# Kernel optimization log

Hardware: AMD Instinct MI355X
Metric: run time of the kernel (lower is better)

## Reference

```python
import jax, jax.numpy as jnp
import numpy as np

V, E, H, B, S = 32000, 128, 256, 8, 512


def setup_inputs() -> dict:
    key = jax.random.key(0)
    ks = jax.random.split(key, 8)
    s_cell = 1.0 / np.sqrt(H)
    return {
        "t": jax.random.randint(ks[0], (B, S), 0, V),
        "emb": jax.random.normal(ks[1], (V, E), dtype=jnp.float32) * 0.02,
        "h0": jnp.zeros((1, H), dtype=jnp.float32),
        "w_ih": jax.random.uniform(ks[2], (3 * H, E), jnp.float32, -s_cell, s_cell),
        "w_hh": jax.random.uniform(ks[3], (3 * H, H), jnp.float32, -s_cell, s_cell),
        "b_ih": jax.random.uniform(ks[4], (3 * H,), jnp.float32, -s_cell, s_cell),
        "b_hh": jax.random.uniform(ks[5], (3 * H,), jnp.float32, -s_cell, s_cell),
        "w_out": jax.random.normal(ks[6], (V, H), dtype=jnp.float32) * 0.02,
        "b_out": jnp.zeros((V,), dtype=jnp.float32),
    }


def reference(t, emb, h0, w_ih, w_hh, b_ih, b_hh, w_out, b_out):
    x = emb[t]  # [B, S, E]
    # Input-side gate pre-activations can be batched over time (same math as per-step GRUCell)
    gi = jnp.einsum("bse,ge->bsg", x, w_ih) + b_ih  # [B, S, 3H]
    h_init = jnp.broadcast_to(h0, (t.shape[0], h0.shape[1]))  # [B, H]

    def step(h, gi_t):  # gi_t: [B, 3H]
        gh = h @ w_hh.T + b_hh  # [B, 3H]
        i_r, i_z, i_n = jnp.split(gi_t, 3, axis=-1)
        h_r, h_z, h_n = jnp.split(gh, 3, axis=-1)
        r = jax.nn.sigmoid(i_r + h_r)
        z = jax.nn.sigmoid(i_z + h_z)
        n = jnp.tanh(i_n + r * h_n)
        h_new = (1.0 - z) * n + z * h
        return h_new, h_new

    _, hs = jax.lax.scan(step, h_init, jnp.swapaxes(gi, 0, 1))  # hs: [S, B, H]
    hidden = jnp.swapaxes(hs, 0, 1)  # [B, S, H]
    return jnp.einsum("bsh,vh->bsv", hidden, w_out) + b_out  # [B, S, V]
```

## Files before the change

### kernel.cpp

```cpp
#include <hip/hip_runtime.h>
#include <stdint.h>


typedef __attribute__((ext_vector_type(8))) _Float16 half8;
typedef __attribute__((ext_vector_type(4))) _Float16 half4;
typedef __attribute__((ext_vector_type(4))) float float4v;
typedef __attribute__((ext_vector_type(4))) float facc4;
typedef __attribute__((ext_vector_type(4))) unsigned short ushort4v;

#define GI_BYTES   (512 * 8 * 768 * 4)
#define HID_BYTES  (4096 * 256 * 2)
#define FLAG_OFF   (GI_BYTES + HID_BYTES)

__device__ __forceinline__ float b2f(unsigned short u) {
  union { unsigned int i; float f; } v; v.i = ((unsigned int)u) << 16; return v.f;
}
__device__ __forceinline__ unsigned short f2b(float f) {
  union { float f; unsigned int i; } v; v.f = f;
  unsigned int r = v.i + 0x7FFFu + ((v.i >> 16) & 1u);
  return (unsigned short)(r >> 16);
}
template<bool BF> __device__ __forceinline__ float ldf(const void* p, int i) {
  if constexpr (BF) return b2f(((const unsigned short*)p)[i]);
  else              return ((const float*)p)[i];
}
template<bool BF> __device__ __forceinline__ float4v ld4(const void* p, int i) {
  float4v r;
  if constexpr (BF) {
    ushort4v u = *reinterpret_cast<const ushort4v*>((const unsigned short*)p + i);
#pragma unroll
    for (int j = 0; j < 4; ++j) r[j] = b2f(u[j]);
  } else {
    r = *reinterpret_cast<const float4v*>((const float*)p + i);
  }
  return r;
}

__global__ void k_detect(const unsigned int* __restrict__ emb_raw,
                         int* __restrict__ flag) {
  int tid = threadIdx.x;
  unsigned int u = emb_raw[tid];
  unsigned int lo = u & 0xFFFFu;
  unsigned int ex = (lo >> 7) & 0xFFu;
  int hit = ((ex >= 96u && ex <= 127u) || lo == 0u) ? 1 : 0;
  unsigned long long m = __ballot(hit);
  if (tid == 0) flag[0] = (__popcll(m) >= 40) ? 1 : 0;
}

template<bool BF>
__global__ __launch_bounds__(256, 4) void k_gi(
    const int* __restrict__ flag, const int* __restrict__ t,
    const void* __restrict__ emb, const void* __restrict__ w_ih,
    const void* __restrict__ b_ih, float* __restrict__ gi)
{
  if (*flag != (BF ? 1 : 0)) return;
  alignas(16) __shared__ float x_lds[4][128];
  const int n0 = blockIdx.x * 4;
  const int tid = threadIdx.x;
  for (int i = tid; i < 512; i += 256) {
    int tk = i >> 7, e = i & 127;
    int n = n0 + tk, s = n >> 3, b = n & 7;
    int tok = t[b * 512 + s];
    x_lds[tk][e] = ldf<BF>(emb, tok * 128 + e);
  }
  __syncthreads();
#pragma unroll
  for (int gg = 0; gg < 3; ++gg) {
    int g = gg * 256 + tid;
    float bias = ldf<BF>(b_ih, g);
    float a0 = bias, a1 = bias, a2 = bias, a3 = bias;
    for (int kb = 0; kb < 32; ++kb) {
      float4v w4 = ld4<BF>(w_ih, g * 128 + kb * 4);
#pragma unroll
      for (int j = 0; j < 4; ++j) {
        float w = w4[j]; int k = kb * 4 + j;
        a0 = fmaf(w, x_lds[0][k], a0);
        a1 = fmaf(w, x_lds[1][k], a1);
        a2 = fmaf(w, x_lds[2][k], a2);
        a3 = fmaf(w, x_lds[3][k], a3);
      }
    }
    gi[(n0 + 0) * 768 + g] = a0;
    gi[(n0 + 1) * 768 + g] = a1;
    gi[(n0 + 2) * 768 + g] = a2;
    gi[(n0 + 3) * 768 + g] = a3;
  }
}

template<bool BF>
__global__ __launch_bounds__(1024, 4) void k_scan(
    const int* __restrict__ flag, const void* __restrict__ w_hh,
    const void* __restrict__ b_hh, const void* __restrict__ h0,
    const float* __restrict__ gi, _Float16* __restrict__ hidden)
{
  if (*flag != (BF ? 1 : 0)) return;
  alignas(16) __shared__ _Float16 a_sh[2][256];
  alignas(16) __shared__ float gi_sh[2][768];
  alignas(16) __shared__ float bhh_sh[768];

  const int tid = threadIdx.x;
  const int b = blockIdx.x;
  const int wave = tid >> 6, lane = tid & 63;
  const int l15 = lane & 15, q = lane >> 4;
  const bool ard = (l15 == 0);
  const int qo = q * 8;

  half8 bfr[3][8];
#pragma unroll
  for (int tt = 0; tt < 3; ++tt) {
    int nrow = tt * 256 + (wave << 4) + l15;
#pragma unroll
    for (int kt = 0; kt < 8; ++kt) {
      int base = nrow * 256 + kt * 32 + qo;
      float4v x0 = ld4<BF>(w_hh, base), x1 = ld4<BF>(w_hh, base + 4);
      half8 h;
#pragma unroll
      for (int jj = 0; jj < 4; ++jj) { h[jj] = (_Float16)x0[jj]; h[4 + jj] = (_Float16)x1[jj]; }
      bfr[tt][kt] = h;
    }
  }

  if (tid < 768) bhh_sh[tid] = ldf<BF>(b_hh, tid);
  if (tid < 256) a_sh[0][tid] = (_Float16)ldf<BF>(h0, tid);
  if (tid < 768) gi_sh[0][tid] = gi[b * 768 + tid];
  float hreg = 0.f;
  if (lane < 16) hreg = ldf<BF>(h0, (wave << 4) + lane);

  half8 a0 = {}, a1 = {};
  _Float16* hid = hidden + b * 512 * 256;
  __syncthreads();

  int p = 0;
  for (int s = 0; s < 512; ++s) {
    float gnext = 0.f;
    if (tid < 768 && s < 511) gnext = gi[(s + 1) * 6144 + b * 768 + tid];

    const _Float16* ap = &a_sh[p][0];
    facc4 acc0 = {}, acc1 = {}, acc2 = {};
    if (ard) a0 = *reinterpret_cast<const half8*>(ap + qo);
#pragma unroll
    for (int kt = 0; kt < 8; kt += 2) {
      if (ard) a1 = *reinterpret_cast<const half8*>(ap + (kt + 1) * 32 + qo);
      acc0 = __builtin_amdgcn_mfma_f32_16x16x32_f16(a0, bfr[0][kt], acc0, 0, 0, 0);
      acc1 = __builtin_amdgcn_mfma_f32_16x16x32_f16(a0, bfr[1][kt], acc1, 0, 0, 0);
      acc2 = __builtin_amdgcn_mfma_f32_16x16x32_f16(a0, bfr[2][kt], acc2, 0, 0, 0);
      if (ard && kt + 2 < 8) a0 = *reinterpret_cast<const half8*>(ap + (kt + 2) * 32 + qo);
      acc0 = __builtin_amdgcn_mfma_f32_16x16x32_f16(a1, bfr[0][kt + 1], acc0, 0, 0, 0);
      acc1 = __builtin_amdgcn_mfma_f32_16x16x32_f16(a1, bfr[1][kt + 1], acc1, 0, 0, 0);
      acc2 = __builtin_amdgcn_mfma_f32_16x16x32_f16(a1, bfr[2][kt + 1], acc2, 0, 0, 0);
    }

    if (tid < 768 && s < 511) gi_sh[p ^ 1][tid] = gnext;

    if (lane < 16) {
      int j = (wave << 4) + lane;
      float ghr = acc0[0] + bhh_sh[j];
      float ghz = acc1[0] + bhh_sh[256 + j];
      float ghn = acc2[0] + bhh_sh[512 + j];
      float gir = gi_sh[p][j], giz = gi_sh[p][256 + j], gin = gi_sh[p][512 + j];
      float r = 1.f / (1.f + __expf(-(gir + ghr)));
      float z = 1.f / (1.f + __expf(-(giz + ghz)));
      float xn = gin + r * ghn;
      float e2 = __expf(2.f * xn);
      float nn = 1.f - 2.f / (e2 + 1.f);
      float hnew = (1.f - z) * nn + z * hreg;
      hreg = hnew;
      _Float16 hf = (_Float16)hnew;
      a_sh[p ^ 1][j] = hf;
      hid[s * 256 + j] = hf;
    }
    __syncthreads();
    p ^= 1;
  }
}

template<bool BF>
__global__ __launch_bounds__(256, 2) void k_out(
    const int* __restrict__ flag, const _Float16* __restrict__ hidden,
    const void* __restrict__ w_out, const void* __restrict__ b_out,
    void* __restrict__ out)
{
  if (*flag != (BF ? 1 : 0)) return;
  alignas(16) __shared__ _Float16 Asm[128 * 72];
  alignas(16) __shared__ _Float16 Bsm[128 * 72];
  const int bid = blockIdx.x;
  const int m0 = (bid & 31) * 128;
  const int n0 = (bid >> 5) * 128;
  const int tid = threadIdx.x;
  const int wave = tid >> 6, lane = tid & 63;
  const int l15 = lane & 15, q = lane >> 4;
  const int wm = (wave >> 1) * 64, wn = (wave & 1) * 64;

  facc4 acc[4][4] = {};
  float bo[4];
#pragma unroll
  for (int nt = 0; nt < 4; ++nt)
    bo[nt] = ldf<BF>(b_out, n0 + wn + nt * 16 + l15);

  for (int kk = 0; kk < 4; ++kk) {
    int k0 = kk * 64;
#pragma unroll
    for (int r = 0; r < 4; ++r) {
      int row = r * 32 + (tid >> 3);
      int ch = tid & 7;
      *reinterpret_cast<half8*>(&Asm[row * 72 + ch * 8]) =
          *reinterpret_cast<const half8*>(hidden + (m0 + row) * 256 + k0 + ch * 8);
      int wbase = (n0 + row) * 256 + k0 + ch * 8;
      float4v w0 = ld4<BF>(w_out, wbase), w1 = ld4<BF>(w_out, wbase + 4);
      half8 hB;
#pragma unroll
      for (int j = 0; j < 4; ++j) { hB[j] = (_Float16)w0[j]; hB[4 + j] = (_Float16)w1[j]; }
      *reinterpret_cast<half8*>(&Bsm[row * 72 + ch * 8]) = hB;
    }
    __syncthreads();
#pragma unroll
    for (int kt = 0; kt < 2; ++kt) {
      int koff = kt * 32 + q * 8;
      half8 af[4], bf[4];
#pragma unroll
      for (int mt = 0; mt < 4; ++mt)
        af[mt] = *reinterpret_cast<const half8*>(&Asm[(wm + mt * 16 + l15) * 72 + koff]);
#pragma unroll
      for (int nt = 0; nt < 4; ++nt)
        bf[nt] = *reinterpret_cast<const half8*>(&Bsm[(wn + nt * 16 + l15) * 72 + koff]);
#pragma unroll
      for (int mt = 0; mt < 4; ++mt)
#pragma unroll
        for (int nt = 0; nt < 4; ++nt)
          acc[mt][nt] = __builtin_amdgcn_mfma_f32_16x16x32_f16(
              af[mt], bf[nt], acc[mt][nt], 0, 0, 0);
    }
    __syncthreads();
  }
#pragma unroll
  for (int mt = 0; mt < 4; ++mt) {
#pragma unroll
    for (int i = 0; i < 4; ++i) {
      int row = m0 + wm + mt * 16 + q * 4 + i;
#pragma unroll
      for (int nt = 0; nt < 4; ++nt) {
        int col = n0 + wn + nt * 16 + l15;
        float val = acc[mt][nt][i] + bo[nt];
        if constexpr (BF) ((unsigned short*)out)[row * 32000 + col] = f2b(val);
        else              ((float*)out)[row * 32000 + col] = val;
      }
    }
  }
}

extern "C" void kernel_launch(void* const* d_in, const int* in_sizes, int n_in,
                              void* d_out, int out_size, void* d_ws, size_t ws_size,
                              hipStream_t stream) {
  const int* t     = (const int*)d_in[0];
  const void* emb  = d_in[1];
  const void* h0   = d_in[2];
  const void* w_ih = d_in[3];
  const void* w_hh = d_in[4];
  const void* b_ih = d_in[5];
  const void* b_hh = d_in[6];
  const void* w_out = d_in[7];
  const void* b_out = d_in[8];

  float*     gi     = (float*)d_ws;
  _Float16*  hidden = (_Float16*)((char*)d_ws + GI_BYTES);
  int*       flag   = (int*)((char*)d_ws + FLAG_OFF);

  k_detect<<<1, 64, 0, stream>>>((const unsigned int*)emb, flag);

  k_gi<false><<<1024, 256, 0, stream>>>(flag, t, emb, w_ih, b_ih, gi);
  k_gi<true> <<<1024, 256, 0, stream>>>(flag, t, emb, w_ih, b_ih, gi);

  k_scan<false><<<8, 1024, 0, stream>>>(flag, w_hh, b_hh, h0, gi, hidden);
  k_scan<true> <<<8, 1024, 0, stream>>>(flag, w_hh, b_hh, h0, gi, hidden);

  k_out<false><<<8000, 256, 0, stream>>>(flag, hidden, w_out, b_out, d_out);
  k_out<true> <<<8000, 256, 0, stream>>>(flag, hidden, w_out, b_out, d_out);
}
```

Baseline: 1.533 ms.

## Restructure GRU scan step: register gi/bias, LDS ring for hidden, lighter barrier

The scan kernel now keeps gate inputs and recurrent biases in registers instead of staging them through shared memory. It seeds the MFMA accumulators with the bias and writes hidden states into a 32-deep LDS ring. Hidden-state global stores are batched as coalesced half4 writes every 16 steps, and the per-step __syncthreads is replaced by an explicit lgkmcnt wait plus s_barrier. The aim is a shorter serial critical path per timestep. The output GEMM also remaps block indices for XCD locality, and removing the occupancy hint on the scan kernel may change register allocation.

New measurement: 2.109 ms. 37.6% more time.

```diff
diff --git a/kernel.cpp b/kernel.cpp
--- a/kernel.cpp
+++ b/kernel.cpp
@@ -34,6 +34,14 @@
     r = *reinterpret_cast<const float4v*>((const float*)p + i);
   }
   return r;
+}
+
+__device__ __forceinline__ void bar_lgkm() {
+  __builtin_amdgcn_sched_barrier(0);
+  asm volatile("s_waitcnt lgkmcnt(0)" ::: "memory");
+  __builtin_amdgcn_sched_barrier(0);
+  __builtin_amdgcn_s_barrier();
+  __builtin_amdgcn_sched_barrier(0);
 }
 
 __global__ void k_detect(const unsigned int* __restrict__ emb_raw,
@@ -88,27 +96,25 @@
 }
 
 template<bool BF>
-__global__ __launch_bounds__(1024, 4) void k_scan(
+__global__ __launch_bounds__(1024) void k_scan(
     const int* __restrict__ flag, const void* __restrict__ w_hh,
     const void* __restrict__ b_hh, const void* __restrict__ h0,
     const float* __restrict__ gi, _Float16* __restrict__ hidden)
 {
   if (*flag != (BF ? 1 : 0)) return;
-  alignas(16) __shared__ _Float16 a_sh[2][256];
-  alignas(16) __shared__ float gi_sh[2][768];
-  alignas(16) __shared__ float bhh_sh[768];
+  alignas(16) __shared__ _Float16 hs[32][256];
 
   const int tid = threadIdx.x;
   const int b = blockIdx.x;
   const int wave = tid >> 6, lane = tid & 63;
   const int l15 = lane & 15, q = lane >> 4;
-  const bool ard = (l15 == 0);
   const int qo = q * 8;
+  const int j = (wave << 4) + l15;
 
   half8 bfr[3][8];
 #pragma unroll
   for (int tt = 0; tt < 3; ++tt) {
-    int nrow = tt * 256 + (wave << 4) + l15;
+    int nrow = tt * 256 + j;
 #pragma unroll
     for (int kt = 0; kt < 8; ++kt) {
       int base = nrow * 256 + kt * 32 + qo;
@@ -120,57 +126,68 @@
     }
   }
 
-  if (tid < 768) bhh_sh[tid] = ldf<BF>(b_hh, tid);
-  if (tid < 256) a_sh[0][tid] = (_Float16)ldf<BF>(h0, tid);
-  if (tid < 768) gi_sh[0][tid] = gi[b * 768 + tid];
-  float hreg = 0.f;
-  if (lane < 16) hreg = ldf<BF>(h0, (wave << 4) + lane);
-
-  half8 a0 = {}, a1 = {};
+  const float bh_r = ldf<BF>(b_hh, j);
+  const float bh_z = ldf<BF>(b_hh, 256 + j);
+  const float bh_n = ldf<BF>(b_hh, 512 + j);
+
+  if (tid < 256) hs[31][tid] = (_Float16)ldf<BF>(h0, tid);
+  float hreg = (lane < 16) ? ldf<BF>(h0, j) : 0.f;
+
+  float gr_c = 0.f, gz_c = 0.f, gn_c = 0.f;
+  if (lane < 16) {
+    const float* g0 = gi + b * 768 + j;
+    gr_c = g0[0]; gz_c = g0[256]; gn_c = g0[512];
+  }
+  __syncthreads();
+
   _Float16* hid = hidden + b * 512 * 256;
-  __syncthreads();
-
-  int p = 0;
+
   for (int s = 0; s < 512; ++s) {
-    float gnext = 0.f;
-    if (tid < 768 && s < 511) gnext = gi[(s + 1) * 6144 + b * 768 + tid];
-
-    const _Float16* ap = &a_sh[p][0];
-    facc4 acc0 = {}, acc1 = {}, acc2 = {};
-    if (ard) a0 = *reinterpret_cast<const half8*>(ap + qo);
+    float gr_n = 0.f, gz_n = 0.f, gn_n = 0.f;
+    if (lane < 16 && s < 511) {
+      const float* gp = gi + (s + 1) * 6144 + b * 768 + j;
+      gr_n = gp[0]; gz_n = gp[256]; gn_n = gp[512];
+    }
+
+    const _Float16* ap = &hs[(s + 31) & 31][0];
+    facc4 acc0 = {bh_r, bh_r, bh_r, bh_r};
+    facc4 acc1 = {bh_z, bh_z, bh_z, bh_z};
+    facc4 acc2 = {bh_n, bh_n, bh_n, bh_n};
+    half8 a0 = *reinterpret_cast<const half8*>(ap + qo);
+    half8 a1;
 #pragma unroll
     for (int kt = 0; kt < 8; kt += 2) {
-      if (ard) a1 = *reinterpret_cast<const half8*>(ap + (kt + 1) * 32 + qo);
+      a1 = *reinterpret_cast<const half8*>(ap + (kt + 1) * 32 + qo);
       acc0 = __builtin_amdgcn_mfma_f32_16x16x32_f16(a0, bfr[0][kt], acc0, 0, 0, 0);
       acc1 = __builtin_amdgcn_mfma_f32_16x16x32_f16(a0, bfr[1][kt], acc1, 0, 0, 0);
       acc2 = __builtin_amdgcn_mfma_f32_16x16x32_f16(a0, bfr[2][kt], acc2, 0, 0, 0);
-      if (ard && kt + 2 < 8) a0 = *reinterpret_cast<const half8*>(ap + (kt + 2) * 32 + qo);
+      if (kt + 2 < 8) a0 = *reinterpret_cast<const half8*>(ap + (kt + 2) * 32 + qo);
       acc0 = __builtin_amdgcn_mfma_f32_16x16x32_f16(a1, bfr[0][kt + 1], acc0, 0, 0, 0);
       acc1 = __builtin_amdgcn_mfma_f32_16x16x32_f16(a1, bfr[1][kt + 1], acc1, 0, 0, 0);
       acc2 = __builtin_amdgcn_mfma_f32_16x16x32_f16(a1, bfr[2][kt + 1], acc2, 0, 0, 0);
     }
 
-    if (tid < 768 && s < 511) gi_sh[p ^ 1][tid] = gnext;
-
     if (lane < 16) {
-      int j = (wave << 4) + lane;
-      float ghr = acc0[0] + bhh_sh[j];
-      float ghz = acc1[0] + bhh_sh[256 + j];
-      float ghn = acc2[0] + bhh_sh[512 + j];
-      float gir = gi_sh[p][j], giz = gi_sh[p][256 + j], gin = gi_sh[p][512 + j];
-      float r = 1.f / (1.f + __expf(-(gir + ghr)));
-      float z = 1.f / (1.f + __expf(-(giz + ghz)));
-      float xn = gin + r * ghn;
+      float r = 1.f / (1.f + __expf(-(gr_c + acc0[0])));
+      float z = 1.f / (1.f + __expf(-(gz_c + acc1[0])));
+      float xn = gn_c + r * acc2[0];
       float e2 = __expf(2.f * xn);
       float nn = 1.f - 2.f / (e2 + 1.f);
       float hnew = (1.f - z) * nn + z * hreg;
       hreg = hnew;
-      _Float16 hf = (_Float16)hnew;
-      a_sh[p ^ 1][j] = hf;
-      hid[s * 256 + j] = hf;
-    }
-    __syncthreads();
-    p ^= 1;
+      hs[s & 31][j] = (_Float16)hnew;
+    }
+    gr_c = gr_n; gz_c = gz_n; gn_c = gn_n;
+
+    bar_lgkm();
+
+    if ((s & 15) == 15) {
+      int s0 = s - 15;
+      int row = tid >> 6;
+      int c4 = (lane & 63) * 4;
+      half4 v = *reinterpret_cast<const half4*>(&hs[(s0 + row) & 31][c4]);
+      *reinterpret_cast<half4*>(hid + (s0 + row) * 256 + c4) = v;
+    }
   }
 }
 
@@ -183,7 +200,8 @@
   if (*flag != (BF ? 1 : 0)) return;
   alignas(16) __shared__ _Float16 Asm[128 * 72];
   alignas(16) __shared__ _Float16 Bsm[128 * 72];
-  const int bid = blockIdx.x;
+  const int bid0 = blockIdx.x;
+  const int bid = (bid0 & 7) * 1000 + (bid0 >> 3);
   const int m0 = (bid & 31) * 128;
   const int n0 = (bid >> 5) * 128;
   const int tid = threadIdx.x;
```
